# Kernel optimization log

Measured on AMD Instinct MI355X. Metric: run time of the kernel, lower is better.

Reference implementation:

```python
import jax, jax.numpy as jnp
import numpy as np

INP_MODES = (8, 8, 8, 8)
OUT_MODES = (8, 8, 8, 8)
TT_RANK = (1, 16, 16, 16, 1)


def _glorot_core(key, shape, tt_shape, tt_rank):
    # glorot-style variance over the full matrix it represents
    n_in = int(np.prod(tt_shape[0]))
    n_out = int(np.prod(tt_shape[1]))
    lamb = 2.0 / (n_in + n_out)
    d = len(tt_shape[0])
    cr_exp = -1.0 / (2 * d)
    var = float(np.prod(np.array(tt_rank, dtype=np.float64) ** cr_exp)) * np.sqrt(lamb)
    return jax.random.normal(key, shape, dtype=jnp.float32) * jnp.float32(var)


def setup_inputs() -> dict:
    key = jax.random.key(0)
    ks = jax.random.split(key, 6)
    x = jax.random.normal(ks[0], (16384, int(np.prod(INP_MODES))), dtype=jnp.float32)
    cores = []
    for k in range(4):
        shape = (TT_RANK[k], INP_MODES[k], OUT_MODES[k], TT_RANK[k + 1])
        cores.append(_glorot_core(ks[k + 1], shape, (INP_MODES, OUT_MODES), TT_RANK))
    b = jnp.ones((1,), dtype=jnp.float32)  # self.b = Parameter(torch.ones(1))
    return {"x": x, "core0": cores[0], "core1": cores[1], "core2": cores[2],
            "core3": cores[3], "b": b}


def tt_matmul(x, cores):
    # x: [B, prod(inp_modes)]; cores[k]: [r_k, i_k, j_k, r_{k+1}]
    bsz = x.shape[0]
    d = len(cores)
    inp_modes = [c.shape[1] for c in cores]
    # t: [B, J_acc, r, i_k * rest]
    t = x.reshape(bsz, 1, 1, -1)
    for k, G in enumerate(cores):
        rest = int(np.prod(inp_modes[k + 1:])) if k + 1 < d else 1
        t = t.reshape(bsz, -1, G.shape[0], G.shape[1], rest)
        # contract rank r and input mode i with core -> new output mode j, rank s
        t = jnp.einsum('bqrim,rijs->bqjsm', t, G)
        # fold j into the accumulated output modes
        B, Q, J, S, M = t.shape
        t = t.reshape(bsz, Q * J, S, M)
    return t.reshape(bsz, -1)  # final rank = 1, rest = 1


def reference(x, core0, core1, core2, core3, b):
    h = tt_matmul(x, [core0, core1, core2, core3]) + b
    return jax.nn.relu(h)
```

## Files before the change

### kernel.cpp

```cpp
#include <hip/hip_runtime.h>

#define MM 16384
#define NN 4096
#define KK 4096
#define BM 256
#define BN 256
#define BK 64
#define NT (KK / BK)

typedef __attribute__((ext_vector_type(8))) unsigned short u16x8;
typedef __attribute__((ext_vector_type(8))) short s16x8;
typedef __attribute__((ext_vector_type(4))) float f32x4;

typedef __attribute__((address_space(1))) const void global_cvoid;
typedef __attribute__((address_space(3))) void lds_void;

__device__ __forceinline__ unsigned short f2bf(float f) {
    unsigned int u = __float_as_uint(f);
    u += 0x7fffu + ((u >> 16) & 1u);
    return (unsigned short)(u >> 16);
}

__device__ __forceinline__ void lds_load16(const void* g, void* l) {
    __builtin_amdgcn_global_load_lds((global_cvoid*)g, (lds_void*)l, 16, 0, 0);
}

__device__ __forceinline__ void mfma16(f32x4& d, s16x8 a, s16x8 b) {
    d = __builtin_amdgcn_mfma_f32_16x16x32_bf16(a, b, d, 0, 0, 0);
}

__global__ void k_build_w01(const float* __restrict__ g0, const float* __restrict__ g1,
                            float* __restrict__ w01) {
    int t = blockIdx.x * 256 + threadIdx.x;
    int s2  = t & 15;
    int j01 = (t >> 4) & 63;
    int i01 = t >> 10;
    int i0 = i01 >> 3, i1 = i01 & 7, j0 = j01 >> 3, j1 = j01 & 7;
    float acc = 0.f;
#pragma unroll
    for (int s1 = 0; s1 < 16; ++s1)
        acc += g0[i0 * 128 + j0 * 16 + s1] * g1[s1 * 1024 + i1 * 128 + j1 * 16 + s2];
    w01[t] = acc;
}

__global__ void k_build_w23(const float* __restrict__ g2, const float* __restrict__ g3,
                            float* __restrict__ w23) {
    int t = blockIdx.x * 256 + threadIdx.x;
    int i23 = t & 63;
    int s2  = (t >> 6) & 15;
    int j23 = t >> 10;
    int i2 = i23 >> 3, i3 = i23 & 7, j2 = j23 >> 3, j3 = j23 & 7;
    float acc = 0.f;
#pragma unroll
    for (int s3 = 0; s3 < 16; ++s3)
        acc += g2[s2 * 1024 + i2 * 128 + j2 * 16 + s3] * g3[s3 * 64 + i3 * 8 + j3];
    w23[t] = acc;
}

__global__ void k_build_wt(const float* __restrict__ w01, const float* __restrict__ w23,
                           unsigned short* __restrict__ wt) {
    unsigned int t = blockIdx.x * 256u + threadIdx.x;
    int k = t & 4095;
    int n = t >> 12;
    int i01 = k >> 6, i23 = k & 63, j01 = n >> 6, j23 = n & 63;
    float acc = 0.f;
#pragma unroll
    for (int s2 = 0; s2 < 16; ++s2)
        acc += w01[i01 * 1024 + j01 * 16 + s2] * w23[j23 * 1024 + s2 * 64 + i23];
    wt[t] = f2bf(acc);
}

__global__ void k_convert(const float* __restrict__ x, unsigned short* __restrict__ xb) {
    size_t i = ((size_t)blockIdx.x * 256 + threadIdx.x) * 8;
    const float4* p = (const float4*)(x + i);
    float4 a = p[0], b = p[1];
    u16x8 o;
    o[0] = f2bf(a.x); o[1] = f2bf(a.y); o[2] = f2bf(a.z); o[3] = f2bf(a.w);
    o[4] = f2bf(b.x); o[5] = f2bf(b.y); o[6] = f2bf(b.z); o[7] = f2bf(b.w);
    *(u16x8*)(xb + i) = o;
}

__global__ __launch_bounds__(512, 2) void k_gemm8(const unsigned short* __restrict__ A,
                                                  const unsigned short* __restrict__ Bt,
                                                  float* __restrict__ C,
                                                  const float* __restrict__ bias) {
    __shared__ unsigned short As[2][BM * BK];
    __shared__ unsigned short Bs[2][BN * BK];

    const int t = threadIdx.x;
    const int lane = t & 63;
    const int w = t >> 6;
    const int wm = w >> 2;
    const int wn = w & 3;

    const int mb = blockIdx.x >> 4;
    const int nb = blockIdx.x & 15;
    const int m0 = mb * BM, n0 = nb * BN;

    const unsigned short* gA[2];
    const unsigned short* gB[2];
    int ldsA[2], ldsB[2];
#pragma unroll
    for (int u = 0; u < 2; ++u) {
        int v = t + u * 512;
        int rowA = (v >> 9) * 128 + ((v & 511) >> 3);
        int cbA = ((v & 7) * 16) ^ ((rowA & 7) << 4);
        gA[u] = A + (size_t)(m0 + rowA) * KK + (cbA >> 1);
        ldsA[u] = rowA * 64 + (v & 7) * 8;
        int rowB = (v >> 8) * 64 + ((v & 255) >> 3);
        int cbB = ((v & 7) * 16) ^ ((rowB & 7) << 4);
        gB[u] = Bt + (size_t)(n0 + rowB) * KK + (cbB >> 1);
        ldsB[u] = rowB * 64 + (v & 7) * 8;
    }

    auto stageA = [&](int tile, int mq, int bsel) {
        int tt = tile < NT ? tile : NT - 1;
#pragma unroll
        for (int u = 0; u < 2; ++u)
            lds_load16(gA[u] + (size_t)mq * 64 * KK + tt * 64,
                       &As[bsel][mq * 4096 + ldsA[u]]);
    };
    auto stageB = [&](int tile, int nq, int bsel) {
        int tt = tile < NT ? tile : NT - 1;
#pragma unroll
        for (int u = 0; u < 2; ++u)
            lds_load16(gB[u] + (size_t)nq * 32 * KK + tt * 64,
                       &Bs[bsel][nq * 2048 + ldsB[u]]);
    };

    const int arb = wm * 128 + (lane & 15);
    const int brb = wn * 64 + (lane & 15);
    const int sw = (lane & 7) << 4;
    const int k0e = ((((lane >> 4) * 16)) ^ sw) >> 1;
    const int k1e = ((((lane >> 4) * 16) + 64) ^ sw) >> 1;

    f32x4 acc[8][4];
#pragma unroll
    for (int i = 0; i < 8; ++i)
#pragma unroll
        for (int j = 0; j < 4; ++j) {
            f32x4 z = {0.f, 0.f, 0.f, 0.f};
            acc[i][j] = z;
        }

    s16x8 a[4][2], b[2][2][2];

    auto KTILE = [&](int ti, int bf) {
        const unsigned short* pA = &As[bf][arb * 64];
        const unsigned short* pB = &Bs[bf][brb * 64];

#pragma unroll
        for (int mf = 0; mf < 4; ++mf) {
            a[mf][0] = *(const s16x8*)(pA + mf * 1024 + k0e);
            a[mf][1] = *(const s16x8*)(pA + mf * 1024 + k1e);
        }
#pragma unroll
        for (int nf = 0; nf < 2; ++nf) {
            b[0][nf][0] = *(const s16x8*)(pB + nf * 1024 + k0e);
            b[0][nf][1] = *(const s16x8*)(pB + nf * 1024 + k1e);
        }
        stageA(ti + 1, 1, bf ^ 1);
        __builtin_amdgcn_s_barrier();
        __builtin_amdgcn_s_setprio(1);
#pragma unroll
        for (int k = 0; k < 2; ++k)
#pragma unroll
            for (int mf = 0; mf < 4; ++mf)
#pragma unroll
                for (int nf = 0; nf < 2; ++nf)
                    mfma16(acc[mf][nf], a[mf][k], b[0][nf][k]);
        __builtin_amdgcn_s_setprio(0);

#pragma unroll
        for (int nf = 0; nf < 2; ++nf) {
            b[1][nf][0] = *(const s16x8*)(pB + 2048 + nf * 1024 + k0e);
            b[1][nf][1] = *(const s16x8*)(pB + 2048 + nf * 1024 + k1e);
        }
        stageA(ti + 2, 0, bf);
        __builtin_amdgcn_s_barrier();
        __builtin_amdgcn_s_setprio(1);
#pragma unroll
        for (int k = 0; k < 2; ++k)
#pragma unroll
            for (int mf = 0; mf < 4; ++mf)
#pragma unroll
                for (int nf = 0; nf < 2; ++nf)
                    mfma16(acc[mf][2 + nf], a[mf][k], b[1][nf][k]);
        __builtin_amdgcn_s_setprio(0);

#pragma unroll
        for (int mf = 0; mf < 4; ++mf) {
            a[mf][0] = *(const s16x8*)(pA + 4096 + mf * 1024 + k0e);
            a[mf][1] = *(const s16x8*)(pA + 4096 + mf * 1024 + k1e);
        }
        stageB(ti + 2, 0, bf);
        __builtin_amdgcn_s_barrier();
        __builtin_amdgcn_s_setprio(1);
#pragma unroll
        for (int k = 0; k < 2; ++k)
#pragma unroll
            for (int mf = 0; mf < 4; ++mf)
#pragma unroll
                for (int nf = 0; nf < 2; ++nf)
                    mfma16(acc[4 + mf][nf], a[mf][k], b[0][nf][k]);
        __builtin_amdgcn_s_setprio(0);

        stageB(ti + 2, 1, bf);
        asm volatile("s_waitcnt vmcnt(6)" ::: "memory");
        __builtin_amdgcn_s_barrier();
        __builtin_amdgcn_s_setprio(1);
#pragma unroll
        for (int k = 0; k < 2; ++k)
#pragma unroll
            for (int mf = 0; mf < 4; ++mf)
#pragma unroll
                for (int nf = 0; nf < 2; ++nf)
                    mfma16(acc[4 + mf][2 + nf], a[mf][k], b[1][nf][k]);
        __builtin_amdgcn_s_setprio(0);
    };

    stageA(0, 0, 0); stageB(0, 0, 0); stageB(0, 1, 0); stageA(0, 1, 0);
    stageA(1, 0, 1); stageB(1, 0, 1); stageB(1, 1, 1);
    asm volatile("s_waitcnt vmcnt(6)" ::: "memory");
    __builtin_amdgcn_s_barrier();

    for (int ti = 0; ti < NT; ti += 2) {
        KTILE(ti, 0);
        KTILE(ti + 1, 1);
    }

    asm volatile("s_waitcnt vmcnt(0)" ::: "memory");
    __builtin_amdgcn_s_barrier();

    const float bias_v = bias[0];
    const int r0 = (lane >> 4) * 4;
    const int cc = lane & 15;
#pragma unroll
    for (int mf = 0; mf < 8; ++mf) {
        const int grow = m0 + wm * 128 + mf * 16 + r0;
#pragma unroll
        for (int nf = 0; nf < 4; ++nf) {
            const int gcol = n0 + wn * 64 + nf * 16 + cc;
            f32x4 v = acc[mf][nf];
            float* cp = C + (size_t)grow * NN + gcol;
#pragma unroll
            for (int r = 0; r < 4; ++r) {
                float o = v[r] + bias_v;
                cp[(size_t)r * NN] = o > 0.f ? o : 0.f;
            }
        }
    }
}

__global__ __launch_bounds__(256) void k_gemm_fb(const float* __restrict__ Af,
                                                 const unsigned short* __restrict__ Bt,
                                                 float* __restrict__ C,
                                                 const float* __restrict__ bias) {
    __shared__ unsigned short As[2][128 * 32];
    __shared__ unsigned short Bs[2][128 * 32];

    const int t = threadIdx.x;
    const int l = t & 63;
    const int w = t >> 6;
    const int wm = w >> 1, wn = w & 1;
    const int lrow = l & 15, lk = l >> 4;

    const int nb = blockIdx.x & 31;
    const int mb = blockIdx.x >> 5;
    const int m0 = mb * 128, n0 = nb * 128;

    f32x4 acc[4][4];
#pragma unroll
    for (int i = 0; i < 4; ++i)
#pragma unroll
        for (int j = 0; j < 4; ++j) {
            f32x4 z = {0.f, 0.f, 0.f, 0.f};
            acc[i][j] = z;
        }

    auto stageB = [&](int kt, int buf) {
#pragma unroll
        for (int q = 0; q < 2; ++q) {
            int c = w * 2 + q;
            int row = c * 16 + (l >> 2);
            int kc = (l & 3) * 8;
            const unsigned short* g = Bt + (size_t)(n0 + row) * KK + kt * 32 + kc;
            lds_load16(g, &Bs[buf][c * 512 + l * 8]);
        }
    };
    auto stageA = [&](int kt, int buf) {
        int row = t >> 1;
        int kh = (t & 1) * 16;
        const float4* g = (const float4*)(Af + (size_t)(m0 + row) * KK + kt * 32 + kh);
        float4 v0 = g[0], v1 = g[1], v2 = g[2], v3 = g[3];
        u16x8 o0, o1;
        o0[0] = f2bf(v0.x); o0[1] = f2bf(v0.y); o0[2] = f2bf(v0.z); o0[3] = f2bf(v0.w);
        o0[4] = f2bf(v1.x); o0[5] = f2bf(v1.y); o0[6] = f2bf(v1.z); o0[7] = f2bf(v1.w);
        o1[0] = f2bf(v2.x); o1[1] = f2bf(v2.y); o1[2] = f2bf(v2.z); o1[3] = f2bf(v2.w);
        o1[4] = f2bf(v3.x); o1[5] = f2bf(v3.y); o1[6] = f2bf(v3.z); o1[7] = f2bf(v3.w);
        *(u16x8*)&As[buf][row * 32 + kh] = o0;
        *(u16x8*)&As[buf][row * 32 + kh + 8] = o1;
    };

    stageA(0, 0);
    stageB(0, 0);

    const int NK = KK / 32;
    for (int kt = 0; kt < NK; ++kt) {
        __syncthreads();
        if (kt + 1 < NK) {
            stageA(kt + 1, (kt + 1) & 1);
            stageB(kt + 1, (kt + 1) & 1);
        }
        const int buf = kt & 1;
        const unsigned short* Ab = &As[buf][(wm * 64 + lrow) * 32 + lk * 8];
        const unsigned short* Bb = &Bs[buf][(wn * 64 + lrow) * 32 + lk * 8];
        s16x8 af[4], bfr[4];
#pragma unroll
        for (int i = 0; i < 4; ++i) af[i] = *(const s16x8*)(Ab + i * 16 * 32);
#pragma unroll
        for (int i = 0; i < 4; ++i) bfr[i] = *(const s16x8*)(Bb + i * 16 * 32);
#pragma unroll
        for (int i = 0; i < 4; ++i)
#pragma unroll
            for (int j = 0; j < 4; ++j) mfma16(acc[i][j], af[i], bfr[j]);
    }

    const float bias_v = bias[0];
    float* Cbase = C + (size_t)m0 * NN + n0;
#pragma unroll
    for (int mi = 0; mi < 4; ++mi) {
        int row0 = wm * 64 + mi * 16 + lk * 4;
#pragma unroll
        for (int ni = 0; ni < 4; ++ni) {
            int col = wn * 64 + ni * 16 + lrow;
            f32x4 v = acc[mi][ni];
#pragma unroll
            for (int r = 0; r < 4; ++r) {
                float o = v[r] + bias_v;
                Cbase[(size_t)(row0 + r) * NN + col] = o > 0.f ? o : 0.f;
            }
        }
    }
}

extern "C" void kernel_launch(void* const* d_in, const int* in_sizes, int n_in,
                              void* d_out, int out_size, void* d_ws, size_t ws_size,
                              hipStream_t stream) {
    const float* x  = (const float*)d_in[0];
    const float* g0 = (const float*)d_in[1];
    const float* g1 = (const float*)d_in[2];
    const float* g2 = (const float*)d_in[3];
    const float* g3 = (const float*)d_in[4];
    const float* bv = (const float*)d_in[5];
    float* out = (float*)d_out;
    char* ws = (char*)d_ws;

    unsigned short* wt = (unsigned short*)(ws);
    float* w01 = (float*)(ws + 33554432);
    float* w23 = (float*)(ws + 33554432 + 262144);
    unsigned short* xb = (unsigned short*)(ws + 34078720);
    const size_t need_full = 34078720ull + (size_t)MM * KK * 2;

    k_build_w01<<<dim3(256), dim3(256), 0, stream>>>(g0, g1, w01);
    k_build_w23<<<dim3(256), dim3(256), 0, stream>>>(g2, g3, w23);
    k_build_wt<<<dim3(65536), dim3(256), 0, stream>>>(w01, w23, wt);

    if (ws_size >= need_full) {
        k_convert<<<dim3(32768), dim3(256), 0, stream>>>(x, xb);
        k_gemm8<<<dim3((MM / BM) * (NN / BN)), dim3(512), 0, stream>>>(xb, wt, out, bv);
    } else {
        k_gemm_fb<<<dim3((MM / 128) * (NN / 128)), dim3(256), 0, stream>>>(x, wt, out, bv);
    }
}
```

Measured before the change: 626.3 us.

## Fuse weight-build kernels and merge W build with x conversion; reschedule A staging

Merges the two small factor-building kernels into one launch, and folds the full bf16 weight construction into the x-to-bf16 conversion kernel with two outputs per thread. This cuts kernel launches and adds more work per thread in the memory-bound conversion. Separately, the GEMM main loop moves the second A half-tile prefetch later and raises the vmcnt wait threshold to match, which changes how loads overlap with MFMA work.

```diff
diff --git a/kernel.cpp b/kernel.cpp
--- a/kernel.cpp
+++ b/kernel.cpp
@@ -29,32 +29,32 @@
     d = __builtin_amdgcn_mfma_f32_16x16x32_bf16(a, b, d, 0, 0, 0);
 }
 
-__global__ void k_build_w01(const float* __restrict__ g0, const float* __restrict__ g1,
-                            float* __restrict__ w01) {
-    int t = blockIdx.x * 256 + threadIdx.x;
-    int s2  = t & 15;
-    int j01 = (t >> 4) & 63;
-    int i01 = t >> 10;
-    int i0 = i01 >> 3, i1 = i01 & 7, j0 = j01 >> 3, j1 = j01 & 7;
-    float acc = 0.f;
-#pragma unroll
-    for (int s1 = 0; s1 < 16; ++s1)
-        acc += g0[i0 * 128 + j0 * 16 + s1] * g1[s1 * 1024 + i1 * 128 + j1 * 16 + s2];
-    w01[t] = acc;
-}
-
-__global__ void k_build_w23(const float* __restrict__ g2, const float* __restrict__ g3,
-                            float* __restrict__ w23) {
-    int t = blockIdx.x * 256 + threadIdx.x;
-    int i23 = t & 63;
-    int s2  = (t >> 6) & 15;
-    int j23 = t >> 10;
-    int i2 = i23 >> 3, i3 = i23 & 7, j2 = j23 >> 3, j3 = j23 & 7;
-    float acc = 0.f;
-#pragma unroll
-    for (int s3 = 0; s3 < 16; ++s3)
-        acc += g2[s2 * 1024 + i2 * 128 + j2 * 16 + s3] * g3[s3 * 64 + i3 * 8 + j3];
-    w23[t] = acc;
+__global__ void k_build_w0123(const float* __restrict__ g0, const float* __restrict__ g1,
+                              const float* __restrict__ g2, const float* __restrict__ g3,
+                              float* __restrict__ w01, float* __restrict__ w23) {
+    int b = blockIdx.x;
+    int t = (b & 255) * 256 + threadIdx.x;
+    if (b < 256) {
+        int s2  = t & 15;
+        int j01 = (t >> 4) & 63;
+        int i01 = t >> 10;
+        int i0 = i01 >> 3, i1 = i01 & 7, j0 = j01 >> 3, j1 = j01 & 7;
+        float acc = 0.f;
+#pragma unroll
+        for (int s1 = 0; s1 < 16; ++s1)
+            acc += g0[i0 * 128 + j0 * 16 + s1] * g1[s1 * 1024 + i1 * 128 + j1 * 16 + s2];
+        w01[t] = acc;
+    } else {
+        int i23 = t & 63;
+        int s2  = (t >> 6) & 15;
+        int j23 = t >> 10;
+        int i2 = i23 >> 3, i3 = i23 & 7, j2 = j23 >> 3, j3 = j23 & 7;
+        float acc = 0.f;
+#pragma unroll
+        for (int s3 = 0; s3 < 16; ++s3)
+            acc += g2[s2 * 1024 + i2 * 128 + j2 * 16 + s3] * g3[s3 * 64 + i3 * 8 + j3];
+        w23[t] = acc;
+    }
 }
 
 __global__ void k_build_wt(const float* __restrict__ w01, const float* __restrict__ w23,
@@ -70,14 +70,31 @@
     wt[t] = f2bf(acc);
 }
 
-__global__ void k_convert(const float* __restrict__ x, unsigned short* __restrict__ xb) {
-    size_t i = ((size_t)blockIdx.x * 256 + threadIdx.x) * 8;
+__global__ void k_wt_convert(const float* __restrict__ w01, const float* __restrict__ w23,
+                             unsigned short* __restrict__ wt,
+                             const float* __restrict__ x, unsigned short* __restrict__ xb) {
+    unsigned int T = blockIdx.x * 256u + threadIdx.x;
+    size_t i = (size_t)T * 8;
     const float4* p = (const float4*)(x + i);
     float4 a = p[0], b = p[1];
     u16x8 o;
     o[0] = f2bf(a.x); o[1] = f2bf(a.y); o[2] = f2bf(a.z); o[3] = f2bf(a.w);
     o[4] = f2bf(b.x); o[5] = f2bf(b.y); o[6] = f2bf(b.z); o[7] = f2bf(b.w);
     *(u16x8*)(xb + i) = o;
+
+    unsigned int t0 = T * 2u;
+    int k = t0 & 4095;
+    int n = t0 >> 12;
+    int i01 = k >> 6, i23 = k & 63, j01 = n >> 6, j23 = n & 63;
+    float acc0 = 0.f, acc1 = 0.f;
+#pragma unroll
+    for (int s2 = 0; s2 < 16; ++s2) {
+        float wa = w01[i01 * 1024 + j01 * 16 + s2];
+        const float* wb = w23 + j23 * 1024 + s2 * 64 + i23;
+        acc0 += wa * wb[0];
+        acc1 += wa * wb[1];
+    }
+    ((unsigned int*)wt)[T] = (unsigned int)f2bf(acc0) | ((unsigned int)f2bf(acc1) << 16);
 }
 
 __global__ __launch_bounds__(512, 2) void k_gemm8(const unsigned short* __restrict__ A,
@@ -159,7 +176,6 @@
             b[0][nf][0] = *(const s16x8*)(pB + nf * 1024 + k0e);
             b[0][nf][1] = *(const s16x8*)(pB + nf * 1024 + k1e);
         }
-        stageA(ti + 1, 1, bf ^ 1);
         __builtin_amdgcn_s_barrier();
         __builtin_amdgcn_s_setprio(1);
 #pragma unroll
@@ -206,7 +222,8 @@
         __builtin_amdgcn_s_setprio(0);
 
         stageB(ti + 2, 1, bf);
-        asm volatile("s_waitcnt vmcnt(6)" ::: "memory");
+        stageA(ti + 2, 1, bf);
+        asm volatile("s_waitcnt vmcnt(8)" ::: "memory");
         __builtin_amdgcn_s_barrier();
         __builtin_amdgcn_s_setprio(1);
 #pragma unroll
@@ -220,8 +237,8 @@
     };
 
     stageA(0, 0, 0); stageB(0, 0, 0); stageB(0, 1, 0); stageA(0, 1, 0);
-    stageA(1, 0, 1); stageB(1, 0, 1); stageB(1, 1, 1);
-    asm volatile("s_waitcnt vmcnt(6)" ::: "memory");
+    stageA(1, 0, 1); stageB(1, 0, 1); stageB(1, 1, 1); stageA(1, 1, 1);
+    asm volatile("s_waitcnt vmcnt(8)" ::: "memory");
     __builtin_amdgcn_s_barrier();
 
     for (int ti = 0; ti < NT; ti += 2) {
@@ -362,14 +379,13 @@
     unsigned short* xb = (unsigned short*)(ws + 34078720);
     const size_t need_full = 34078720ull + (size_t)MM * KK * 2;
 
-    k_build_w01<<<dim3(256), dim3(256), 0, stream>>>(g0, g1, w01);
-    k_build_w23<<<dim3(256), dim3(256), 0, stream>>>(g2, g3, w23);
-    k_build_wt<<<dim3(65536), dim3(256), 0, stream>>>(w01, w23, wt);
+    k_build_w0123<<<dim3(512), dim3(256), 0, stream>>>(g0, g1, g2, g3, w01, w23);
 
     if (ws_size >= need_full) {
-        k_convert<<<dim3(32768), dim3(256), 0, stream>>>(x, xb);
+        k_wt_convert<<<dim3(32768), dim3(256), 0, stream>>>(w01, w23, wt, x, xb);
         k_gemm8<<<dim3((MM / BM) * (NN / BN)), dim3(512), 0, stream>>>(xb, wt, out, bv);
     } else {
+        k_build_wt<<<dim3(65536), dim3(256), 0, stream>>>(w01, w23, wt);
         k_gemm_fb<<<dim3((MM / 128) * (NN / 128)), dim3(256), 0, stream>>>(x, wt, out, bv);
     }
 }
```

After: 620.2 us. Within noise of the previous version (-1.0%).
